# Kernel tuning notes

Hardware: AMD Instinct MI355X
Metric: run time of the kernel (lower is better)

## Reference

```python
import jax, jax.numpy as jnp
import numpy as np

DIM = 1024
EXPERT_DIM = 2048
N_EXPERTS = 2
B, T = 4, 2048


def setup_inputs() -> dict:
    key = jax.random.key(0)
    ks = jax.random.split(key, 10)
    s = 0.02
    return {
        "x": jax.random.normal(ks[0], (B, T, DIM), dtype=jnp.float32),
        "W_router": jax.random.normal(ks[1], (DIM, N_EXPERTS), dtype=jnp.float32) * s,
        "router_bias": jnp.zeros((N_EXPERTS,), dtype=jnp.float32),
        "Wg": jax.random.normal(ks[2], (N_EXPERTS, DIM, EXPERT_DIM), dtype=jnp.float32) * s,
        "Wu": jax.random.normal(ks[3], (N_EXPERTS, DIM, EXPERT_DIM), dtype=jnp.float32) * s,
        "Wd": jax.random.normal(ks[4], (N_EXPERTS, EXPERT_DIM, DIM), dtype=jnp.float32) * s,
        "Sg": jax.random.normal(ks[5], (DIM, EXPERT_DIM), dtype=jnp.float32) * s,
        "Su": jax.random.normal(ks[6], (DIM, EXPERT_DIM), dtype=jnp.float32) * s,
        "Sd": jax.random.normal(ks[7], (EXPERT_DIM, DIM), dtype=jnp.float32) * s,
    }


def reference(x, W_router, router_bias, Wg, Wu, Wd, Sg, Su, Sd):
    Bc, Tc, D = x.shape
    flat = x.reshape(Bc * Tc, D)                               # [N, D]
    logits = flat @ W_router                                   # [N, E]
    scores = jax.nn.softmax(logits, axis=-1)
    hard = jax.nn.one_hot(jnp.argmax(logits + router_bias, axis=-1),
                          W_router.shape[1], dtype=flat.dtype)  # [N, E]
    # straight-through weights: forward value == hard, grad flows via scores
    ste = hard + scores - jax.lax.stop_gradient(scores)
    w = jnp.where(hard > 0.5, ste, jnp.zeros_like(ste))         # mask w > 0.5 (== argmax expert)
    # routed SwiGLU experts (top-1 hard routing; unselected rows weighted 0)
    g = jax.nn.silu(jnp.einsum('nd,edf->enf', flat, Wg))        # [E, N, F]
    u = jnp.einsum('nd,edf->enf', flat, Wu)
    y = jnp.einsum('enf,efd->end', g * u, Wd)                   # [E, N, D]
    routed = jnp.einsum('ne,end->nd', w, y)                     # [N, D]
    # always-active shared SwiGLU expert
    shared = (jax.nn.silu(flat @ Sg) * (flat @ Su)) @ Sd        # [N, D]
    return (routed + shared).reshape(Bc, Tc, D)
```

## Files before the change

kernel.cpp:

```cpp
#include <hip/hip_runtime.h>
#include <stdint.h>

#define NTOK 8192
#define DIM 1024
#define EDIM 2048

typedef __attribute__((ext_vector_type(8))) short bf16x8;
typedef __attribute__((ext_vector_type(4))) float f32x4;

__device__ __forceinline__ unsigned short f2bf(float f) {
  union { float f; unsigned u; } v; v.f = f;
  unsigned r = (v.u + 0x7FFF + ((v.u >> 16) & 1)) >> 16;
  return (unsigned short)r;
}

__device__ __forceinline__ void gload16(const void* g, void* l) {
  __builtin_amdgcn_global_load_lds(
      (const __attribute__((address_space(1))) unsigned int*)g,
      (__attribute__((address_space(3))) unsigned int*)l, 16, 0, 0);
}

__global__ void pre_k(const float* __restrict__ x, const float* __restrict__ Wr,
                      const float* __restrict__ bias,
                      const float* __restrict__ Sg, const float* __restrict__ Su,
                      const float* __restrict__ Sd, const float* __restrict__ Wg,
                      const float* __restrict__ Wu, const float* __restrict__ Wd,
                      unsigned short* __restrict__ xb, int* __restrict__ choice,
                      unsigned short* __restrict__ wt) {
  const int bx = blockIdx.x;
  const int t = threadIdx.x;
  const size_t MSZ = (size_t)DIM * EDIM;
  if (bx < 1024) {
    const int wid = t >> 6, lane = t & 63;
    const float b0 = bias[0], b1 = bias[1];
    const float2* wr = (const float2*)Wr;
    #pragma unroll
    for (int r = 0; r < 2; ++r) {
      const int n = bx * 8 + wid * 2 + r;
      const float4* xr = (const float4*)(x + (size_t)n * DIM);
      uint2* xo = (uint2*)(xb + (size_t)n * DIM);
      float s0 = 0.f, s1 = 0.f;
      #pragma unroll
      for (int i = 0; i < 4; ++i) {
        const int idx = i * 64 + lane;
        float4 v = xr[idx];
        float2 wa = wr[idx * 4], wb = wr[idx * 4 + 1], wc = wr[idx * 4 + 2], wd = wr[idx * 4 + 3];
        s0 += v.x * wa.x + v.y * wb.x + v.z * wc.x + v.w * wd.x;
        s1 += v.x * wa.y + v.y * wb.y + v.z * wc.y + v.w * wd.y;
        union { unsigned short s[4]; uint2 u; } o;
        o.s[0] = f2bf(v.x); o.s[1] = f2bf(v.y); o.s[2] = f2bf(v.z); o.s[3] = f2bf(v.w);
        xo[idx] = o.u;
      }
      #pragma unroll
      for (int off = 32; off; off >>= 1) {
        s0 += __shfl_xor(s0, off);
        s1 += __shfl_xor(s1, off);
      }
      if (lane == 0) choice[n] = (s1 + b1 > s0 + b0) ? 1 : 0;
    }
    return;
  }
  const int id = bx - 1024;
  const int mat = id >> 11;
  const int tile = id & 2047;
  const float* src; unsigned short* dst; int type;
  switch (mat) {
    case 0: src = Sg;       dst = wt;            type = 0; break;
    case 1: src = Su;       dst = wt;            type = 1; break;
    case 2: src = Wg;       dst = wt + 4194304;  type = 0; break;
    case 3: src = Wu;       dst = wt + 4194304;  type = 1; break;
    case 4: src = Wg + MSZ; dst = wt + 8388608;  type = 0; break;
    case 5: src = Wu + MSZ; dst = wt + 8388608;  type = 1; break;
    case 6: src = Sd;       dst = wt + 12582912; type = 2; break;
    case 7: src = Wd;       dst = wt + 14680064; type = 2; break;
    default: src = Wd + MSZ; dst = wt + 16777216; type = 2; break;
  }
  const int R = (type == 2) ? EDIM : DIM;
  const int C = (type == 2) ? DIM : EDIM;
  __shared__ float ts[32][33];
  const int tC = C >> 5;
  const int tr = tile / tC, tc = tile % tC;
  const int xt = t & 31, yt = t >> 5;
  #pragma unroll
  for (int j = 0; j < 4; ++j)
    ts[yt + j * 8][xt] = src[(size_t)(tr * 32 + yt + j * 8) * C + tc * 32 + xt];
  __syncthreads();
  #pragma unroll
  for (int j = 0; j < 4; ++j) {
    const int cc = tc * 32 + yt + j * 8;
    const int rr = tr * 32 + xt;
    const float v = ts[xt][yt + j * 8];
    if (type == 2) dst[(size_t)cc * EDIM + rr] = f2bf(v);
    else {
      const int row = ((cc >> 4) << 5) + (cc & 15) + (type << 4);
      dst[(size_t)row * DIM + rr] = f2bf(v);
    }
  }
}

__global__ void scan_k(const int* __restrict__ choice, int* __restrict__ counts,
                       int* __restrict__ rowlist) {
  const int t = threadIdx.x;
  const int base = t * 8;
  int c[8]; int ones = 0;
  #pragma unroll
  for (int j = 0; j < 8; ++j) { c[j] = choice[base + j]; ones += c[j]; }
  const int lane = t & 63, wid = t >> 6;
  int v = ones;
  #pragma unroll
  for (int off = 1; off < 64; off <<= 1) {
    int o = __shfl_up(v, off);
    if (lane >= off) v += o;
  }
  __shared__ int wsum[16];
  if (lane == 63) wsum[wid] = v;
  __syncthreads();
  int pre = 0, tot = 0;
  #pragma unroll
  for (int w = 0; w < 16; ++w) {
    int s = wsum[w];
    if (w < wid) pre += s;
    tot += s;
  }
  const int excl = pre + v - ones;
  const int cnt0 = NTOK - tot;
  int p0 = base - excl;
  int p1 = cnt0 + excl;
  #pragma unroll
  for (int j = 0; j < 8; ++j) {
    if (c[j]) rowlist[p1++] = base + j;
    else rowlist[p0++] = base + j;
  }
  if (t == 0) { counts[0] = cnt0; counts[1] = tot; }
}

template<int KDIM, int MODE>
__global__ __launch_bounds__(256, 4)
void gemm2_k(const unsigned short* __restrict__ A, const unsigned short* __restrict__ B0,
             const int* __restrict__ counts, const int* __restrict__ rl,
             unsigned short* __restrict__ h, float* __restrict__ out) {
  constexpr int NT = KDIM / 64;
  constexpr int ROWB = KDIM * 2;

  int e = 0, mstart = 0, cntE = NTOK, r0;
  if (MODE == 1 || MODE == 3) {
    e = blockIdx.x >> 6;
    const int mt = blockIdx.x & 63;
    const int c0 = counts[0];
    cntE = e ? (NTOK - c0) : c0;
    mstart = e ? c0 : 0;
    r0 = mt * 128;
    if (r0 >= cntE) return;
  } else {
    r0 = blockIdx.x * 128;
  }
  const int n0 = blockIdx.y * 128;
  const unsigned short* B = B0;
  if (MODE == 1) B += (size_t)e * 4194304u;
  if (MODE == 3) B += (size_t)e * 2097152u;

  __shared__ __align__(16) unsigned char lA[16384];
  __shared__ __align__(16) unsigned char lB[16384];

  const int t = threadIdx.x;
  const int lane = t & 63;
  const int wm = t >> 7, wn = (t >> 6) & 1;
  const int l15 = lane & 15, l4 = lane >> 4;

  size_t aoff[4]; uint32_t boff[4]; int dsto[4];
  #pragma unroll
  for (int i = 0; i < 4; ++i) {
    const int flat = i * 4096 + t * 16;
    const int row = flat >> 7;
    const int kb = (flat & 127) ^ ((row & 7) << 4);
    int ar;
    if (MODE == 1) {
      int idx = r0 + row; if (idx >= cntE) idx = cntE - 1;
      ar = rl[mstart + idx];
    } else if (MODE == 3) {
      int idx = r0 + row; if (idx >= cntE) idx = cntE - 1;
      ar = mstart + idx;
    } else {
      ar = r0 + row;
    }
    aoff[i] = (size_t)ar * ROWB + kb;
    boff[i] = (uint32_t)(n0 + row) * ROWB + kb;
    dsto[i] = flat;
  }

  f32x4 acc[4][4];
  #pragma unroll
  for (int i = 0; i < 4; ++i)
    #pragma unroll
    for (int j = 0; j < 4; ++j) acc[i][j] = f32x4{0.f, 0.f, 0.f, 0.f};

  const char* Ab = (const char*)A;
  const char* Bb = (const char*)B;

  for (int kt = 0; kt < NT; ++kt) {
    __syncthreads();
    const size_t ko = (size_t)kt * 128;
    #pragma unroll
    for (int i = 0; i < 4; ++i) {
      gload16(Ab + aoff[i] + ko, lA + dsto[i]);
      gload16(Bb + boff[i] + ko, lB + dsto[i]);
    }
    __syncthreads();
    #pragma unroll
    for (int ks = 0; ks < 2; ++ks) {
      bf16x8 af[4], bf[4];
      const int kb = ks * 64 + (l4 << 4);
      #pragma unroll
      for (int mi = 0; mi < 4; ++mi) {
        const int row = wm * 64 + mi * 16 + l15;
        af[mi] = *(const bf16x8*)(lA + row * 128 + (kb ^ ((row & 7) << 4)));
      }
      #pragma unroll
      for (int ni = 0; ni < 4; ++ni) {
        const int col = wn * 64 + ni * 16 + l15;
        bf[ni] = *(const bf16x8*)(lB + col * 128 + (kb ^ ((col & 7) << 4)));
      }
      #pragma unroll
      for (int mi = 0; mi < 4; ++mi)
        #pragma unroll
        for (int ni = 0; ni < 4; ++ni)
          acc[mi][ni] = __builtin_amdgcn_mfma_f32_16x16x32_bf16(af[mi], bf[ni], acc[mi][ni], 0, 0, 0);
    }
  }

  #pragma unroll
  for (int mi = 0; mi < 4; ++mi) {
    #pragma unroll
    for (int r = 0; r < 4; ++r) {
      const int rit = wm * 64 + mi * 16 + l4 * 4 + r;
      if (MODE == 0 || MODE == 1) {
        const int pos = r0 + rit;
        if (MODE == 1 && pos >= cntE) continue;
        unsigned short* hr = h + (size_t)(mstart + pos) * EDIM;
        const int f0 = (n0 >> 1) + wn * 32;
        #pragma unroll
        for (int j = 0; j < 2; ++j) {
          const float g = acc[mi][2 * j][r], u = acc[mi][2 * j + 1][r];
          hr[f0 + j * 16 + l15] = f2bf(g / (1.f + __expf(-g)) * u);
        }
      } else if (MODE == 2) {
        float* orow = out + (size_t)(r0 + rit) * DIM;
        #pragma unroll
        for (int n = 0; n < 4; ++n)
          orow[n0 + wn * 64 + n * 16 + l15] = acc[mi][n][r];
      } else {
        const int pos = r0 + rit;
        if (pos >= cntE) continue;
        const int tok = rl[mstart + pos];
        float* orow = out + (size_t)tok * DIM;
        #pragma unroll
        for (int n = 0; n < 4; ++n)
          orow[n0 + wn * 64 + n * 16 + l15] += acc[mi][n][r];
      }
    }
  }
}

extern "C" void kernel_launch(void* const* d_in, const int* in_sizes, int n_in,
                              void* d_out, int out_size, void* d_ws, size_t ws_size,
                              hipStream_t stream) {
  const float* x  = (const float*)d_in[0];
  const float* Wr = (const float*)d_in[1];
  const float* rb = (const float*)d_in[2];
  const float* Wg = (const float*)d_in[3];
  const float* Wu = (const float*)d_in[4];
  const float* Wd = (const float*)d_in[5];
  const float* Sg = (const float*)d_in[6];
  const float* Su = (const float*)d_in[7];
  const float* Sd = (const float*)d_in[8];
  float* out = (float*)d_out;

  char* ws = (char*)d_ws;
  int* counts  = (int*)ws;
  int* choice  = (int*)(ws + 256);
  int* rowlist = (int*)(ws + 256 + 32768);
  unsigned short* xb = (unsigned short*)(ws + 256 + 65536);
  unsigned short* wt = xb + (size_t)NTOK * DIM;
  unsigned short* h  = wt + 18874368;

  const unsigned short* Sgu  = wt;
  const unsigned short* Wgu0 = wt + 4194304;
  const unsigned short* Sdt  = wt + 12582912;
  const unsigned short* Wdt0 = wt + 14680064;

  pre_k<<<1024 + 9 * 2048, 256, 0, stream>>>(x, Wr, rb, Sg, Su, Sd, Wg, Wu, Wd,
                                             xb, choice, wt);
  scan_k<<<1, 1024, 0, stream>>>(choice, counts, rowlist);

  gemm2_k<DIM, 0><<<dim3(64, 32), 256, 0, stream>>>(xb, Sgu, counts, rowlist, h, nullptr);
  gemm2_k<EDIM, 2><<<dim3(64, 8), 256, 0, stream>>>(h, Sdt, counts, rowlist, nullptr, out);
  gemm2_k<DIM, 1><<<dim3(128, 32), 256, 0, stream>>>(xb, Wgu0, counts, rowlist, h, nullptr);
  gemm2_k<EDIM, 3><<<dim3(128, 8), 256, 0, stream>>>(h, Wdt0, counts, rowlist, nullptr, out);
}
```

Before: 280.3 us.

## Add 256x256-tile 8-wave up-projection GEMM with phased LDS pipeline

Replaces the 128x128 gate/up GEMMs (shared and routed) with a new 512-thread kernel using 256x256 output tiles, quad-buffered LDS, and a four-phase schedule that interleaves async global-to-LDS loads with MFMA work and raises wave priority around the MFMAs. The gate/up weight interleave is changed from 16-column to 64-column groups to match the new tile's column mapping. The larger tile is meant to raise arithmetic intensity and overlap memory with compute, at the cost of more registers and LDS, fewer blocks, and more padding waste on partial routed tiles.

```diff
diff --git a/kernel.cpp b/kernel.cpp
--- a/kernel.cpp
+++ b/kernel.cpp
@@ -19,6 +19,9 @@
       (const __attribute__((address_space(1))) unsigned int*)g,
       (__attribute__((address_space(3))) unsigned int*)l, 16, 0, 0);
 }
+
+#define BARRIER() do { __builtin_amdgcn_s_barrier(); asm volatile("" ::: "memory"); } while (0)
+#define VMW(n) asm volatile("s_waitcnt vmcnt(" #n ")" ::: "memory")
 
 __global__ void pre_k(const float* __restrict__ x, const float* __restrict__ Wr,
                       const float* __restrict__ bias,
@@ -75,7 +78,6 @@
     case 7: src = Wd;       dst = wt + 14680064; type = 2; break;
     default: src = Wd + MSZ; dst = wt + 16777216; type = 2; break;
   }
-  const int R = (type == 2) ? EDIM : DIM;
   const int C = (type == 2) ? DIM : EDIM;
   __shared__ float ts[32][33];
   const int tC = C >> 5;
@@ -92,7 +94,7 @@
     const float v = ts[xt][yt + j * 8];
     if (type == 2) dst[(size_t)cc * EDIM + rr] = f2bf(v);
     else {
-      const int row = ((cc >> 4) << 5) + (cc & 15) + (type << 4);
+      const int row = ((cc >> 6) << 7) + (cc & 63) + (type << 6);
       dst[(size_t)row * DIM + rr] = f2bf(v);
     }
   }
@@ -132,6 +134,145 @@
     else rowlist[p0++] = base + j;
   }
   if (t == 0) { counts[0] = cnt0; counts[1] = tot; }
+}
+
+template<bool GATHER>
+__global__ __launch_bounds__(512, 2)
+void up8_k(const unsigned short* __restrict__ A, const unsigned short* __restrict__ Bgu,
+           const int* __restrict__ counts, const int* __restrict__ rl,
+           unsigned short* __restrict__ h) {
+  constexpr int NT = DIM / 64;
+  int e = 0, mstart = 0, cntE = NTOK, r0;
+  if (GATHER) {
+    e = blockIdx.x >> 5;
+    const int mt = blockIdx.x & 31;
+    const int c0 = counts[0];
+    cntE = e ? (NTOK - c0) : c0;
+    mstart = e ? c0 : 0;
+    r0 = mt * 256;
+    if (r0 >= cntE) return;
+  } else r0 = blockIdx.x * 256;
+  const int n0 = blockIdx.y * 256;
+  const unsigned short* Bp = Bgu + (GATHER ? (size_t)e * 4194304u : 0u);
+
+  __shared__ __align__(16) unsigned char lA[4][16384];
+  __shared__ __align__(16) unsigned char lB[4][16384];
+
+  const int t = threadIdx.x, lane = t & 63, wid = t >> 6;
+  const int wm = wid >> 2, wn = wid & 3;
+  const int l15 = lane & 15, l4 = lane >> 4;
+  const int wml = wm * 16 + l15, wnl = wn * 16 + l15, l4s = l4 << 4;
+  const int t16 = t * 16;
+
+  const int srow = t >> 3;
+  const int skb = ((t & 7) << 4) ^ ((srow & 7) << 4);
+  uint32_t srcA0_0, srcA0_1, srcA1_0, srcA1_1;
+  {
+    int r00 = 0 * 128 + srow, r01 = 0 * 128 + 64 + srow;
+    int r10 = 1 * 128 + srow, r11 = 1 * 128 + 64 + srow;
+    int g00, g01, g10, g11;
+    if (GATHER) {
+      int i0 = r0 + r00; if (i0 >= cntE) i0 = cntE - 1; g00 = rl[mstart + i0];
+      int i1 = r0 + r01; if (i1 >= cntE) i1 = cntE - 1; g01 = rl[mstart + i1];
+      int i2 = r0 + r10; if (i2 >= cntE) i2 = cntE - 1; g10 = rl[mstart + i2];
+      int i3 = r0 + r11; if (i3 >= cntE) i3 = cntE - 1; g11 = rl[mstart + i3];
+    } else { g00 = r0 + r00; g01 = r0 + r01; g10 = r0 + r10; g11 = r0 + r11; }
+    srcA0_0 = (uint32_t)g00 * (DIM * 2) + skb;
+    srcA0_1 = (uint32_t)g01 * (DIM * 2) + skb;
+    srcA1_0 = (uint32_t)g10 * (DIM * 2) + skb;
+    srcA1_1 = (uint32_t)g11 * (DIM * 2) + skb;
+  }
+  const uint32_t srcB0_0 = (uint32_t)(n0 + srow) * (DIM * 2) + skb;
+  const uint32_t srcB0_1 = (uint32_t)(n0 + 64 + srow) * (DIM * 2) + skb;
+  const uint32_t srcB1_0 = (uint32_t)(n0 + 128 + srow) * (DIM * 2) + skb;
+  const uint32_t srcB1_1 = (uint32_t)(n0 + 192 + srow) * (DIM * 2) + skb;
+
+  const char* Ab = (const char*)A;
+  const char* Bb = (const char*)Bp;
+
+#define STAGE_A0(KT, PARI) do { if ((KT) < NT) { char* d_ = (char*)lA[(PARI) * 2 + 0]; \
+  const int ko_ = (KT) * 128; \
+  gload16(Ab + srcA0_0 + ko_, d_ + t16); gload16(Ab + srcA0_1 + ko_, d_ + 8192 + t16); } } while (0)
+#define STAGE_A1(KT, PARI) do { if ((KT) < NT) { char* d_ = (char*)lA[(PARI) * 2 + 1]; \
+  const int ko_ = (KT) * 128; \
+  gload16(Ab + srcA1_0 + ko_, d_ + t16); gload16(Ab + srcA1_1 + ko_, d_ + 8192 + t16); } } while (0)
+#define STAGE_B0(KT, PARI) do { if ((KT) < NT) { char* d_ = (char*)lB[(PARI) * 2 + 0]; \
+  const int ko_ = (KT) * 128; \
+  gload16(Bb + srcB0_0 + ko_, d_ + t16); gload16(Bb + srcB0_1 + ko_, d_ + 8192 + t16); } } while (0)
+#define STAGE_B1(KT, PARI) do { if ((KT) < NT) { char* d_ = (char*)lB[(PARI) * 2 + 1]; \
+  const int ko_ = (KT) * 128; \
+  gload16(Bb + srcB1_0 + ko_, d_ + t16); gload16(Bb + srcB1_1 + ko_, d_ + 8192 + t16); } } while (0)
+
+  f32x4 acc[8][4];
+  #pragma unroll
+  for (int i = 0; i < 8; ++i)
+    #pragma unroll
+    for (int j = 0; j < 4; ++j) acc[i][j] = f32x4{0.f, 0.f, 0.f, 0.f};
+
+  STAGE_A0(0, 0); STAGE_B1(0, 0); STAGE_A1(0, 0); STAGE_B0(0, 0);
+  STAGE_A0(1, 1); STAGE_B1(1, 1);
+  VMW(4);
+  BARRIER();
+
+#define PHASE(RH, CH, STG) do { \
+  const unsigned char* As_ = lA[par2 + (RH)]; \
+  const unsigned char* Bs_ = lB[par2 + (CH)]; \
+  bf16x8 aR[4][2], bR[2][2]; \
+  _Pragma("unroll") for (int m = 0; m < 4; ++m) { \
+    const int r_ = m * 32 + wml; \
+    _Pragma("unroll") for (int k = 0; k < 2; ++k) \
+      aR[m][k] = *(const bf16x8*)(As_ + r_ * 128 + (((k << 6) | l4s) ^ ((r_ & 7) << 4))); \
+  } \
+  _Pragma("unroll") for (int q = 0; q < 2; ++q) { \
+    const int r_ = q * 64 + wnl; \
+    _Pragma("unroll") for (int k = 0; k < 2; ++k) \
+      bR[q][k] = *(const bf16x8*)(Bs_ + r_ * 128 + (((k << 6) | l4s) ^ ((r_ & 7) << 4))); \
+  } \
+  STG; \
+  BARRIER(); \
+  __builtin_amdgcn_s_setprio(1); \
+  _Pragma("unroll") for (int m = 0; m < 4; ++m) \
+    _Pragma("unroll") for (int q = 0; q < 2; ++q) { \
+      acc[4 * (RH) + m][2 * (CH) + q] = __builtin_amdgcn_mfma_f32_16x16x32_bf16( \
+          aR[m][0], bR[q][0], acc[4 * (RH) + m][2 * (CH) + q], 0, 0, 0); \
+      acc[4 * (RH) + m][2 * (CH) + q] = __builtin_amdgcn_mfma_f32_16x16x32_bf16( \
+          aR[m][1], bR[q][1], acc[4 * (RH) + m][2 * (CH) + q], 0, 0, 0); \
+    } \
+  __builtin_amdgcn_s_setprio(0); \
+} while (0)
+
+  for (int kt = 0; kt < NT; ++kt) {
+    const int par2 = (kt & 1) * 2;
+    const int parN = (kt + 1) & 1;
+    PHASE(0, 0, STAGE_A1(kt + 1, parN)); BARRIER();
+    PHASE(0, 1, STAGE_B0(kt + 1, parN)); BARRIER();
+    PHASE(1, 1, STAGE_A0(kt + 2, kt & 1)); BARRIER();
+    PHASE(1, 0, STAGE_B1(kt + 2, kt & 1));
+    if (kt + 2 < NT) { VMW(4); BARRIER(); }
+    else if (kt + 1 < NT) { VMW(0); BARRIER(); }
+  }
+
+  #pragma unroll
+  for (int f = 0; f < 8; ++f) {
+    #pragma unroll
+    for (int rr = 0; rr < 4; ++rr) {
+      const int rit = f * 32 + wm * 16 + l4 * 4 + rr;
+      const int pos = r0 + rit;
+      if (GATHER && pos >= cntE) continue;
+      unsigned short* hr = h + (size_t)(mstart + pos) * EDIM;
+      const int f0 = (n0 >> 1) + wnl;
+      #pragma unroll
+      for (int jp = 0; jp < 2; ++jp) {
+        const float g = acc[f][2 * jp][rr], u = acc[f][2 * jp + 1][rr];
+        hr[f0 + jp * 64] = f2bf(g / (1.f + __expf(-g)) * u);
+      }
+    }
+  }
+#undef PHASE
+#undef STAGE_A0
+#undef STAGE_A1
+#undef STAGE_B0
+#undef STAGE_B1
 }
 
 template<int KDIM, int MODE>
@@ -143,7 +284,7 @@
   constexpr int ROWB = KDIM * 2;
 
   int e = 0, mstart = 0, cntE = NTOK, r0;
-  if (MODE == 1 || MODE == 3) {
+  if (MODE == 3) {
     e = blockIdx.x >> 6;
     const int mt = blockIdx.x & 63;
     const int c0 = counts[0];
@@ -156,7 +297,6 @@
   }
   const int n0 = blockIdx.y * 128;
   const unsigned short* B = B0;
-  if (MODE == 1) B += (size_t)e * 4194304u;
   if (MODE == 3) B += (size_t)e * 2097152u;
 
   __shared__ __align__(16) unsigned char lA[16384];
@@ -174,10 +314,7 @@
     const int row = flat >> 7;
     const int kb = (flat & 127) ^ ((row & 7) << 4);
     int ar;
-    if (MODE == 1) {
-      int idx = r0 + row; if (idx >= cntE) idx = cntE - 1;
-      ar = rl[mstart + idx];
-    } else if (MODE == 3) {
+    if (MODE == 3) {
       int idx = r0 + row; if (idx >= cntE) idx = cntE - 1;
       ar = mstart + idx;
     } else {
@@ -233,17 +370,7 @@
     #pragma unroll
     for (int r = 0; r < 4; ++r) {
       const int rit = wm * 64 + mi * 16 + l4 * 4 + r;
-      if (MODE == 0 || MODE == 1) {
-        const int pos = r0 + rit;
-        if (MODE == 1 && pos >= cntE) continue;
-        unsigned short* hr = h + (size_t)(mstart + pos) * EDIM;
-        const int f0 = (n0 >> 1) + wn * 32;
-        #pragma unroll
-        for (int j = 0; j < 2; ++j) {
-          const float g = acc[mi][2 * j][r], u = acc[mi][2 * j + 1][r];
-          hr[f0 + j * 16 + l15] = f2bf(g / (1.f + __expf(-g)) * u);
-        }
-      } else if (MODE == 2) {
+      if (MODE == 2) {
         float* orow = out + (size_t)(r0 + rit) * DIM;
         #pragma unroll
         for (int n = 0; n < 4; ++n)
@@ -292,8 +419,8 @@
                                              xb, choice, wt);
   scan_k<<<1, 1024, 0, stream>>>(choice, counts, rowlist);
 
-  gemm2_k<DIM, 0><<<dim3(64, 32), 256, 0, stream>>>(xb, Sgu, counts, rowlist, h, nullptr);
+  up8_k<false><<<dim3(32, 16), 512, 0, stream>>>(xb, Sgu, counts, rowlist, h);
   gemm2_k<EDIM, 2><<<dim3(64, 8), 256, 0, stream>>>(h, Sdt, counts, rowlist, nullptr, out);
-  gemm2_k<DIM, 1><<<dim3(128, 32), 256, 0, stream>>>(xb, Wgu0, counts, rowlist, h, nullptr);
+  up8_k<true><<<dim3(64, 16), 512, 0, stream>>>(xb, Wgu0, counts, rowlist, h);
   gemm2_k<EDIM, 3><<<dim3(128, 8), 256, 0, stream>>>(h, Wdt0, counts, rowlist, nullptr, out);
 }
```

Result: slower. 382.7 us (+36.5%).
